# Optimization experiments

Measured on AMD Instinct MI355X. Metric: run time of the kernel, lower is better.

Reference implementation:

```python
import jax, jax.numpy as jnp
import numpy as np

B, S, D, H, L, DFF, NA = 128, 52, 1024, 16, 8, 4096, 1000
DK = D // H
KTOP = int((1.0 - 0.9) * S)  # per-row top-k kept before threshold = 5
EPS = 1e-5
SCALE = 1.0 / np.sqrt(DK).astype(np.float32)


def setup_inputs() -> dict:
    key = jax.random.key(0)
    ks = jax.random.split(key, 30)
    # token grid: channels 0,1 in [0,50) so only designated positions match special tokens
    x = jax.random.randint(ks[0], (B, S, 3), 0, 50).astype(jnp.int32)
    act = jax.random.randint(ks[1], (B, S), 0, NA).astype(jnp.int32)
    x = x.at[..., 2].set(act)
    x = x.at[:, 0].set(jnp.array([100, 0, 1], jnp.int32))    # SOS
    x = x.at[:, 26].set(jnp.array([100, 0, 2], jnp.int32))   # SEP
    x = x.at[:, 48:].set(jnp.array([100, 0, 0], jnp.int32))  # PAD tail

    def n(k, shape, scale=0.02):
        return (jax.random.normal(k, shape) * scale).astype(jnp.float32)

    return dict(
        x=x,
        action_emb=n(ks[2], (NA, D), 1.0),
        sep_token=n(ks[3], (D,), 1.0),
        bn_gamma=jnp.ones((S,), jnp.float32),
        bn_beta=jnp.zeros((S,), jnp.float32),
        Wq=n(ks[4], (L, D, D)), bq=jnp.zeros((L, D), jnp.float32),
        Wk=n(ks[5], (L, D, D)), bk=jnp.zeros((L, D), jnp.float32),
        Wv=n(ks[6], (L, D, D)), bv=jnp.zeros((L, D), jnp.float32),
        Wo=n(ks[7], (L, D, D)), bo=jnp.zeros((L, D), jnp.float32),
        W1=n(ks[8], (L, DFF, D)), b1=jnp.zeros((L, DFF), jnp.float32),
        W2=n(ks[9], (L, D, DFF)), b2=jnp.zeros((L, D), jnp.float32),
        ln1_g=jnp.ones((L, D), jnp.float32), ln1_b=jnp.zeros((L, D), jnp.float32),
        ln2_g=jnp.ones((L, D), jnp.float32), ln2_b=jnp.zeros((L, D), jnp.float32),
        Wout=n(ks[10], (3, D)), bout=jnp.zeros((3,), jnp.float32),
    )


def _ln(x, g, b):
    m = x.mean(-1, keepdims=True)
    v = x.var(-1, keepdims=True)
    return (x - m) * jax.lax.rsqrt(v + EPS) * g + b


def reference(x, action_emb, sep_token, bn_gamma, bn_beta,
              Wq, bq, Wk, bk, Wv, bv, Wo, bo,
              W1, b1, W2, b2, ln1_g, ln1_b, ln2_g, ln2_b, Wout, bout):
    PAD = jnp.array([100, 0, 0], x.dtype)
    SEP = jnp.array([100, 0, 2], x.dtype)
    pad = jnp.all(x == PAD, -1)            # [B,S]
    sep = jnp.all(x == SEP, -1)            # [B,S]
    valid = ~pad                            # attend only to non-pad keys

    # token-scatter embedding: sep positions -> sep_token, everything else -> action embedding
    h = jnp.where(sep[..., None], sep_token, action_emb[x[..., 2]])  # [B,S,D]

    # BatchNorm1d(52) over seq-as-channel dim (training-mode batch stats)
    mu = h.mean((0, 2), keepdims=True)
    var = h.var((0, 2), keepdims=True)
    h = (h - mu) * jax.lax.rsqrt(var + EPS) * bn_gamma[None, :, None] + bn_beta[None, :, None]

    for l in range(L):
        q = (h @ Wq[l].T + bq[l]).reshape(B, S, H, DK).transpose(0, 2, 1, 3)
        k = (h @ Wk[l].T + bk[l]).reshape(B, S, H, DK).transpose(0, 2, 1, 3)
        v = (h @ Wv[l].T + bv[l]).reshape(B, S, H, DK).transpose(0, 2, 1, 3)
        scores = jnp.einsum('bhqd,bhkd->bhqk', q, k) * SCALE       # [B,H,S,S]
        scores = jnp.where(valid[:, None, None, :], scores, -1e9)
        thr = jax.lax.top_k(scores, KTOP)[0][..., -1:]              # per-row k-th largest
        sparse = scores * (scores >= thr).astype(scores.dtype)      # zero out sub-threshold
        attn = jax.nn.softmax(sparse, axis=-1)
        o = jnp.einsum('bhqk,bhkd->bhqd', attn, v).transpose(0, 2, 1, 3).reshape(B, S, D)
        o = o @ Wo[l].T + bo[l]
        h = _ln(h + o, ln1_g[l], ln1_b[l])
        f = jax.nn.relu(h @ W1[l].T + b1[l]) @ W2[l].T + b2[l]
        h = _ln(h + f, ln2_g[l], ln2_b[l])

    y = h @ Wout.T + bout                                           # [B,S,3]
    return y[:, -1]
```

## Files before the change

kernel.cpp:

```cpp
#include <hip/hip_runtime.h>
#include <cstddef>
#include <cstdint>

#define B_    128
#define S_    52
#define D_    1024
#define H_    16
#define L_    8
#define DFF_  4096
#define DK_   64
#define T_    (B_*S_)
#define EPS_  1e-5f
#define SCALE_ 0.125f

typedef unsigned short ushortx4 __attribute__((ext_vector_type(4)));
typedef short  bf16x8 __attribute__((ext_vector_type(8)));
typedef float  f32x4  __attribute__((ext_vector_type(4)));

__device__ __forceinline__ unsigned short f2b(float f) {
  unsigned int u = __builtin_bit_cast(unsigned int, f);
  u = u + 0x7fffu + ((u >> 16) & 1u);
  return (unsigned short)(u >> 16);
}
__device__ __forceinline__ float b2f(unsigned short b) {
  unsigned int u = ((unsigned int)b) << 16;
  return __builtin_bit_cast(float, u);
}
__device__ __forceinline__ void gload16(const void* g, void* l) {
  __builtin_amdgcn_global_load_lds((const __attribute__((address_space(1))) unsigned int*)g,
      (__attribute__((address_space(3))) unsigned int*)l, 16, 0, 0);
}

__global__ __launch_bounds__(256) void k_embed(const int* __restrict__ x,
    const float* __restrict__ aemb, const float* __restrict__ sept,
    float* __restrict__ h, float* __restrict__ part, int* __restrict__ mask)
{
  int row = blockIdx.x;
  int b = row / S_;
  int s = row - b * S_;
  const int* xr = x + (size_t)row * 3;
  int x0 = xr[0], x1 = xr[1], x2 = xr[2];
  bool issep = (x0 == 100) && (x1 == 0) && (x2 == 2);
  bool ispad = (x0 == 100) && (x1 == 0) && (x2 == 0);
  int t = threadIdx.x;
  if (t == 0) mask[row] = ispad ? 0 : 1;
  const float* src = issep ? sept : (aemb + (size_t)x2 * D_);
  size_t base = (size_t)row * D_;
  float s1 = 0.f, s2 = 0.f;
#pragma unroll
  for (int i = 0; i < 4; ++i) {
    int d = t + i * 256;
    float v = src[d];
    h[base + d] = v;
    s1 += v;
    s2 += v * v;
  }
#pragma unroll
  for (int off = 32; off; off >>= 1) {
    s1 += __shfl_down(s1, off);
    s2 += __shfl_down(s2, off);
  }
  __shared__ float red[8];
  int lane = t & 63, wid = t >> 6;
  if (lane == 0) { red[wid] = s1; red[4 + wid] = s2; }
  __syncthreads();
  if (t == 0) {
    part[(size_t)s * B_ + b]        = red[0] + red[1] + red[2] + red[3];
    part[(size_t)(S_ + s) * B_ + b] = red[4] + red[5] + red[6] + red[7];
  }
}

__global__ __launch_bounds__(128) void k_bn_reduce(const float* __restrict__ part,
                                                   float* __restrict__ stats)
{
  int s = blockIdx.x;
  int t = threadIdx.x;
  float s1 = part[(size_t)s * B_ + t];
  float s2 = part[(size_t)(S_ + s) * B_ + t];
#pragma unroll
  for (int off = 32; off; off >>= 1) {
    s1 += __shfl_down(s1, off);
    s2 += __shfl_down(s2, off);
  }
  __shared__ float red[4];
  int lane = t & 63, wid = t >> 6;
  if (lane == 0) { red[wid] = s1; red[2 + wid] = s2; }
  __syncthreads();
  if (t == 0) {
    stats[s]      = red[0] + red[1];
    stats[S_ + s] = red[2] + red[3];
  }
}

__global__ __launch_bounds__(256) void k_bn_apply(float* __restrict__ h,
    const float* __restrict__ stats, const float* __restrict__ g,
    const float* __restrict__ bb, unsigned short* __restrict__ hb)
{
  int row = blockIdx.x;
  int s = row % S_;
  const float cnt = (float)(B_ * D_);
  float mu  = stats[s] / cnt;
  float var = stats[S_ + s] / cnt - mu * mu;
  float sc  = rsqrtf(var + EPS_) * g[s];
  float off = bb[s] - mu * sc;
  size_t base = (size_t)row * D_;
  int t = threadIdx.x;
#pragma unroll
  for (int i = 0; i < 4; ++i) {
    int d = t + i * 256;
    float v = h[base + d] * sc + off;
    h[base + d] = v;
    hb[base + d] = f2b(v);
  }
}

__global__ __launch_bounds__(256) void k_wconv8(
    const float* __restrict__ Wq, const float* __restrict__ Wk,
    const float* __restrict__ Wv, const float* __restrict__ Wo,
    const float* __restrict__ W1, const float* __restrict__ W2,
    unsigned short* __restrict__ out, int nlayers)
{
  const size_t DD = (size_t)D_ * D_;
  const size_t DF = (size_t)DFF_ * D_;
  const size_t per = 4 * DD + 2 * DF;
  const size_t total = per * (size_t)nlayers;
  size_t stride = (size_t)gridDim.x * 256 * 4;
  for (size_t i = ((size_t)blockIdx.x * 256 + threadIdx.x) * 4; i < total; i += stride) {
    size_t lay = i / per;
    size_t j = i - lay * per;
    const float* src; size_t off;
    if      (j < DD)          { src = Wq + lay * DD; off = j; }
    else if (j < 2 * DD)      { src = Wk + lay * DD; off = j - DD; }
    else if (j < 3 * DD)      { src = Wv + lay * DD; off = j - 2 * DD; }
    else if (j < 4 * DD)      { src = Wo + lay * DD; off = j - 3 * DD; }
    else if (j < 4 * DD + DF) { src = W1 + lay * DF; off = j - 4 * DD; }
    else                      { src = W2 + lay * DF; off = j - 4 * DD - DF; }
    float4 v = *reinterpret_cast<const float4*>(src + off);
    ushortx4 o = { f2b(v.x), f2b(v.y), f2b(v.z), f2b(v.w) };
    *reinterpret_cast<ushortx4*>(out + i) = o;
  }
}

__global__ __launch_bounds__(256) void k_bcat(const float* __restrict__ bq,
    const float* __restrict__ bk, const float* __restrict__ bv,
    float* __restrict__ out)
{
  int i = blockIdx.x * 256 + threadIdx.x;
  int l = i / 3072, j = i - l * 3072;
  float v = (j < D_) ? bq[l * D_ + j] : (j < 2 * D_) ? bk[l * D_ + j - D_]
                                                     : bv[l * D_ + j - 2 * D_];
  out[i] = v;
}

template<int RELU, int OUTBF16>
__global__ __launch_bounds__(512, 4) void k_gemm8(
    const unsigned short* __restrict__ A, const unsigned short* __restrict__ Wt,
    const float* __restrict__ bias, void* __restrict__ C,
    int Mtiles, int Ntiles, int K, int ldc)
{
  __shared__ unsigned short lds[3 * 12288];
  const int tid = threadIdx.x;
  const int w = tid >> 6, l = tid & 63;

  const int nwg = Mtiles * Ntiles;
  int id = blockIdx.x;
  int swz = (id & 7) * (nwg >> 3) + (id >> 3);
  const int stripe = swz / (Ntiles << 3);
  const int r = swz - stripe * (Ntiles << 3);
  int hg = Mtiles - (stripe << 3); if (hg > 8) hg = 8;
  const int c = r / (hg << 3);
  const int q = r - c * (hg << 3);
  const int bym = (stripe << 3) + (q >> 3);
  const int bxn = (c << 3) + (q & 7);
  const int bm = bym * 256, bn = bxn * 128;

  const int colsw = 16 * ((l & 3) ^ ((l >> 3) & 3));
  const char* gA = (const char*)A + ((size_t)(bm + w * 32 + (l >> 2)) * K) * 2 + colsw;
  const char* gB = (const char*)Wt + ((size_t)(bn + w * 16 + (l >> 2)) * K) * 2 + colsw;
  const size_t r16 = (size_t)16 * K * 2;
  unsigned short* lA = lds + w * 1024;
  unsigned short* lB = lds + 8192 + w * 512;

#define STAGE(tt, bb) do {                          \
    size_t ko_ = (size_t)(tt) * 64;                 \
    unsigned short* la_ = lA + (bb) * 12288;        \
    unsigned short* lb_ = lB + (bb) * 12288;        \
    gload16(gA + ko_,       la_);                   \
    gload16(gA + ko_ + r16, la_ + 512);             \
    gload16(gB + ko_,       lb_);                   \
  } while (0)

  const int fr = l & 15, kg = l >> 4;
  const int wr = w >> 1, wc = w & 1;
  const int xk = 16 * (kg ^ ((fr >> 1) & 3));
  const int aOff = (wr * 64 + fr) * 64 + xk;
  const int bOff = 16384 + (wc * 64 + fr) * 64 + xk;

  f32x4 acc[4][4] = {};
  const int NT = K >> 5;

  STAGE(0, 0);
  STAGE(1, 1);
  int cur = 0;
  for (int t = 0; t < NT; ++t) {
    if (t + 1 < NT) { asm volatile("s_waitcnt vmcnt(3)" ::: "memory"); }
    else            { asm volatile("s_waitcnt vmcnt(0)" ::: "memory"); }
    __builtin_amdgcn_sched_barrier(0);
    __builtin_amdgcn_s_barrier();
    __builtin_amdgcn_sched_barrier(0);
    if (t + 2 < NT) {
      int nb = cur + 2; if (nb >= 3) nb -= 3;
      STAGE(t + 2, nb);
    }
    const char* bp = (const char*)lds + cur * 24576;
    bf16x8 af[4], bfv[4];
#pragma unroll
    for (int mf = 0; mf < 4; ++mf)
      af[mf] = *(const bf16x8*)(bp + aOff + mf * 1024);
#pragma unroll
    for (int nf = 0; nf < 4; ++nf)
      bfv[nf] = *(const bf16x8*)(bp + bOff + nf * 1024);
    asm volatile("s_waitcnt lgkmcnt(0)" ::: "memory");
    __builtin_amdgcn_sched_barrier(0);
    __builtin_amdgcn_s_setprio(1);
#pragma unroll
    for (int mf = 0; mf < 4; ++mf)
#pragma unroll
      for (int nf = 0; nf < 4; ++nf)
        acc[mf][nf] = __builtin_amdgcn_mfma_f32_16x16x32_bf16(af[mf], bfv[nf], acc[mf][nf], 0, 0, 0);
    __builtin_amdgcn_s_setprio(0);
    __builtin_amdgcn_sched_barrier(0);
    cur = (cur == 2) ? 0 : cur + 1;
  }
#undef STAGE

#pragma unroll
  for (int nf = 0; nf < 4; ++nf) {
    int col = bn + wc * 64 + nf * 16 + fr;
    float bv = bias[col];
#pragma unroll
    for (int mf = 0; mf < 4; ++mf) {
      int row0 = bm + wr * 64 + mf * 16 + kg * 4;
#pragma unroll
      for (int j = 0; j < 4; ++j) {
        float v = acc[mf][nf][j] + bv;
        if (RELU) v = fmaxf(v, 0.f);
        if (OUTBF16)
          ((unsigned short*)C)[(size_t)(row0 + j) * ldc + col] = f2b(v);
        else
          ((float*)C)[(size_t)(row0 + j) * ldc + col] = v;
      }
    }
  }
}

__global__ __launch_bounds__(64) void k_attn(const unsigned short* __restrict__ qkv,
    const int* __restrict__ mask, unsigned short* __restrict__ ao)
{
  __shared__ float sc[64][68];
  __shared__ unsigned short ph[64][68];
  __shared__ unsigned short plo[64][68];
  __shared__ unsigned short vT[64][68];
  __shared__ float dnm[64];

  int blk = blockIdx.x;
  int b = blk >> 4, hh = blk & 15;
  int l = threadIdx.x;
  int cl = l & 15, kg = l >> 4;
  const unsigned short* base = qkv + (size_t)(b * S_) * 3072 + hh * 64;

  {
    const unsigned short* vp = base + 2048 + l;
#pragma unroll 4
    for (int k = 0; k < S_; ++k)
      vT[l][k] = vp[(size_t)k * 3072];
#pragma unroll
    for (int k = S_; k < 64; ++k) vT[l][k] = 0;
  }

  bf16x8 qa[4][2], kb[4][2];
#pragma unroll
  for (int mi = 0; mi < 4; ++mi) {
    int row = mi * 16 + cl;
    bool ok = (row < S_);
    const unsigned short* qp = base + (size_t)row * 3072 + kg * 8;
#pragma unroll
    for (int ks = 0; ks < 2; ++ks) {
      bf16x8 z = {};
      qa[mi][ks] = ok ? *reinterpret_cast<const bf16x8*>(qp + ks * 32) : z;
      kb[mi][ks] = ok ? *reinterpret_cast<const bf16x8*>(qp + 1024 + ks * 32) : z;
    }
  }

  f32x4 acc[4][4] = {};
#pragma unroll
  for (int ks = 0; ks < 2; ++ks)
#pragma unroll
    for (int mi = 0; mi < 4; ++mi)
#pragma unroll
      for (int ci = 0; ci < 4; ++ci)
        acc[mi][ci] = __builtin_amdgcn_mfma_f32_16x16x32_bf16(qa[mi][ks], kb[ci][ks], acc[mi][ci], 0, 0, 0);

  int vld[4];
#pragma unroll
  for (int ci = 0; ci < 4; ++ci) {
    int col = ci * 16 + cl;
    vld[ci] = (col < S_) ? mask[b * S_ + col] : 0;
  }
#pragma unroll
  for (int mi = 0; mi < 4; ++mi)
#pragma unroll
    for (int ci = 0; ci < 4; ++ci)
#pragma unroll
      for (int j = 0; j < 4; ++j)
        sc[mi * 16 + kg * 4 + j][ci * 16 + cl] = vld[ci] ? acc[mi][ci][j] * SCALE_ : -1e9f;

  __syncthreads();

  if (l < S_) {
    float v0 = -3e38f, v1 = -3e38f, v2 = -3e38f, v3 = -3e38f, v4 = -3e38f;
    const float4* rp = reinterpret_cast<const float4*>(&sc[l][0]);
#pragma unroll
    for (int c4 = 0; c4 < 13; ++c4) {
      float4 x = rp[c4];
      float xs[4] = { x.x, x.y, x.z, x.w };
#pragma unroll
      for (int u = 0; u < 4; ++u) {
        float xv = xs[u];
        if      (xv > v0) { v4 = v3; v3 = v2; v2 = v1; v1 = v0; v0 = xv; }
        else if (xv > v1) { v4 = v3; v3 = v2; v2 = v1; v1 = xv; }
        else if (xv > v2) { v4 = v3; v3 = v2; v2 = xv; }
        else if (xv > v3) { v4 = v3; v3 = xv; }
        else if (xv > v4) { v4 = xv; }
      }
    }
    float thr = v4;
    float m = fmaxf(v0, 0.f);
    float denom = 0.f;
    for (int c = 0; c < S_; ++c) {
      float xv = sc[l][c];
      float sp = (xv >= thr) ? xv : 0.f;
      float e = __expf(sp - m);
      denom += e;
      unsigned short hi = f2b(e);
      ph[l][c] = hi;
      plo[l][c] = f2b(e - b2f(hi));
    }
#pragma unroll
    for (int c = S_; c < 64; ++c) { ph[l][c] = 0; plo[l][c] = 0; }
    dnm[l] = 1.f / denom;
  }
  __syncthreads();

  f32x4 o[4][4] = {};
#pragma unroll
  for (int ks = 0; ks < 2; ++ks) {
    bf16x8 vf[4];
#pragma unroll
    for (int di = 0; di < 4; ++di)
      vf[di] = *reinterpret_cast<const bf16x8*>(&vT[di * 16 + cl][ks * 32 + kg * 8]);
#pragma unroll
    for (int mi = 0; mi < 4; ++mi) {
      bf16x8 ahi = *reinterpret_cast<const bf16x8*>(&ph[mi * 16 + cl][ks * 32 + kg * 8]);
      bf16x8 alo = *reinterpret_cast<const bf16x8*>(&plo[mi * 16 + cl][ks * 32 + kg * 8]);
#pragma unroll
      for (int di = 0; di < 4; ++di) {
        o[mi][di] = __builtin_amdgcn_mfma_f32_16x16x32_bf16(ahi, vf[di], o[mi][di], 0, 0, 0);
        o[mi][di] = __builtin_amdgcn_mfma_f32_16x16x32_bf16(alo, vf[di], o[mi][di], 0, 0, 0);
      }
    }
  }

#pragma unroll
  for (int mi = 0; mi < 4; ++mi) {
    int row = mi * 16 + kg * 4;
    if (row < S_) {
#pragma unroll
      for (int j = 0; j < 4; ++j) {
        int r = row + j;
        float inv = dnm[r];
        unsigned short* aop = ao + (size_t)(b * S_ + r) * D_ + hh * DK_;
#pragma unroll
        for (int di = 0; di < 4; ++di)
          aop[di * 16 + cl] = f2b(o[mi][di][j] * inv);
      }
    }
  }
}

__global__ __launch_bounds__(256) void k_add_ln(float* __restrict__ h,
    const float* __restrict__ r, const float* __restrict__ g,
    const float* __restrict__ bb, unsigned short* __restrict__ hb)
{
  int row = blockIdx.x;
  size_t base = (size_t)row * D_;
  int t = threadIdx.x;
  float xs[4];
  float s1 = 0.f, s2 = 0.f;
#pragma unroll
  for (int i = 0; i < 4; ++i) {
    int d = t + i * 256;
    float xv = h[base + d] + r[base + d];
    xs[i] = xv;
    s1 += xv;
    s2 += xv * xv;
  }
#pragma unroll
  for (int off = 32; off; off >>= 1) {
    s1 += __shfl_down(s1, off);
    s2 += __shfl_down(s2, off);
  }
  __shared__ float red[8];
  int lane = t & 63, wid = t >> 6;
  if (lane == 0) { red[wid] = s1; red[4 + wid] = s2; }
  __syncthreads();
  if (t == 0) {
    red[0] = red[0] + red[1] + red[2] + red[3];
    red[4] = red[4] + red[5] + red[6] + red[7];
  }
  __syncthreads();
  float mean = red[0] / (float)D_;
  float var  = red[4] / (float)D_ - mean * mean;
  float inv  = rsqrtf(var + EPS_);
#pragma unroll
  for (int i = 0; i < 4; ++i) {
    int d = t + i * 256;
    float v = (xs[i] - mean) * inv * g[d] + bb[d];
    h[base + d] = v;
    hb[base + d] = f2b(v);
  }
}

__global__ __launch_bounds__(256) void k_final(const float* __restrict__ h,
    const float* __restrict__ Wout, const float* __restrict__ bout,
    float* __restrict__ y)
{
  int b = blockIdx.x;
  const float* hr = h + (size_t)(b * S_ + (S_ - 1)) * D_;
  int t = threadIdx.x;
  float p0 = 0.f, p1 = 0.f, p2 = 0.f;
  for (int d = t; d < D_; d += 256) {
    float xv = hr[d];
    p0 += xv * Wout[d];
    p1 += xv * Wout[D_ + d];
    p2 += xv * Wout[2 * D_ + d];
  }
#pragma unroll
  for (int off = 32; off; off >>= 1) {
    p0 += __shfl_down(p0, off);
    p1 += __shfl_down(p1, off);
    p2 += __shfl_down(p2, off);
  }
  __shared__ float red[12];
  int lane = t & 63, wid = t >> 6;
  if (lane == 0) { red[wid] = p0; red[4 + wid] = p1; red[8 + wid] = p2; }
  __syncthreads();
  if (t == 0) {
    y[b * 3 + 0] = red[0] + red[1] + red[2]  + red[3]  + bout[0];
    y[b * 3 + 1] = red[4] + red[5] + red[6]  + red[7]  + bout[1];
    y[b * 3 + 2] = red[8] + red[9] + red[10] + red[11] + bout[2];
  }
}

extern "C" void kernel_launch(void* const* d_in, const int* in_sizes, int n_in,
                              void* d_out, int out_size, void* d_ws, size_t ws_size,
                              hipStream_t stream)
{
  const int*   x    = (const int*)d_in[0];
  const float* aemb = (const float*)d_in[1];
  const float* sept = (const float*)d_in[2];
  const float* bng  = (const float*)d_in[3];
  const float* bnb  = (const float*)d_in[4];
  const float* Wq = (const float*)d_in[5];  const float* bq = (const float*)d_in[6];
  const float* Wk = (const float*)d_in[7];  const float* bk = (const float*)d_in[8];
  const float* Wv = (const float*)d_in[9];  const float* bv = (const float*)d_in[10];
  const float* Wo = (const float*)d_in[11]; const float* bo = (const float*)d_in[12];
  const float* W1 = (const float*)d_in[13]; const float* b1 = (const float*)d_in[14];
  const float* W2 = (const float*)d_in[15]; const float* b2 = (const float*)d_in[16];
  const float* ln1g = (const float*)d_in[17]; const float* ln1b = (const float*)d_in[18];
  const float* ln2g = (const float*)d_in[19]; const float* ln2b = (const float*)d_in[20];
  const float* Wout = (const float*)d_in[21]; const float* bout = (const float*)d_in[22];
  float* out = (float*)d_out;

  float* ws = (float*)d_ws;
  const size_t TD = (size_t)T_ * D_;
  const size_t DD = (size_t)D_ * D_;
  const size_t DF = (size_t)DFF_ * D_;
  const size_t WPL = 4 * DD + 2 * DF;
  float* h   = ws;
  float* tmp = ws + TD;
  unsigned short* hb   = (unsigned short*)(ws + 2 * TD);
  unsigned short* qkvb = (unsigned short*)(ws + 2 * TD + TD / 2);
  unsigned short* aob  = (unsigned short*)(ws + 4 * TD);
  unsigned short* ffb  = (unsigned short*)(ws + 4 * TD + TD / 2);
  float* bqkv  = ws + 6 * TD + TD / 2;
  float* stats = bqkv + L_ * 3072;
  float* part  = stats + 2 * S_;
  int*   mask  = (int*)(part + 2 * S_ * B_);
  size_t usedB = ((char*)(mask + T_) - (char*)ws + 255) & ~(size_t)255;
  unsigned short* wbuf = (unsigned short*)((char*)ws + usedB);
  const int all8 = (ws_size >= usedB + 8 * WPL * sizeof(unsigned short)) ? 1 : 0;

  k_embed<<<T_, 256, 0, stream>>>(x, aemb, sept, h, part, mask);
  k_bn_reduce<<<S_, 128, 0, stream>>>(part, stats);
  k_bn_apply<<<T_, 256, 0, stream>>>(h, stats, bng, bnb, hb);
  k_bcat<<<(L_ * 3072) / 256, 256, 0, stream>>>(bq, bk, bv, bqkv);
  if (all8)
    k_wconv8<<<4096, 256, 0, stream>>>(Wq, Wk, Wv, Wo, W1, W2, wbuf, L_);

  for (int l = 0; l < L_; ++l) {
    unsigned short* wl = all8 ? (wbuf + (size_t)l * WPL) : wbuf;
    if (!all8)
      k_wconv8<<<3072, 256, 0, stream>>>(Wq + l * DD, Wk + l * DD, Wv + l * DD,
                                         Wo + l * DD, W1 + l * DF, W2 + l * DF, wbuf, 1);
    k_gemm8<0, 1><<<26 * 24, 512, 0, stream>>>(hb, wl, bqkv + l * 3072,
        qkvb, 26, 24, 1024, 3072);
    k_attn<<<B_ * H_, 64, 0, stream>>>(qkvb, mask, aob);
    k_gemm8<0, 0><<<26 * 8, 512, 0, stream>>>(aob, wl + 3 * DD, bo + l * D_,
        tmp, 26, 8, 1024, 1024);
    k_add_ln<<<T_, 256, 0, stream>>>(h, tmp, ln1g + l * D_, ln1b + l * D_, hb);
    k_gemm8<1, 1><<<26 * 32, 512, 0, stream>>>(hb, wl + 4 * DD, b1 + l * DFF_,
        ffb, 26, 32, 1024, 4096);
    k_gemm8<0, 0><<<26 * 8, 512, 0, stream>>>(ffb, wl + 4 * DD + DF, b2 + l * D_,
        tmp, 26, 8, 4096, 1024);
    k_add_ln<<<T_, 256, 0, stream>>>(h, tmp, ln2g + l * D_, ln2b + l * D_, hb);
  }
  k_final<<<B_, 256, 0, stream>>>(h, Wout, bout, out);
}
```

Measured before the change: 2.438 ms.

## Add 256x256 tiled pipelined GEMM for QKV and FFN1; split weight conversion by segment

```diff
diff --git a/kernel.cpp b/kernel.cpp
--- a/kernel.cpp
+++ b/kernel.cpp
@@ -114,30 +114,30 @@
   }
 }
 
-__global__ __launch_bounds__(256) void k_wconv8(
+__global__ __launch_bounds__(256) void k_wconv6(
     const float* __restrict__ Wq, const float* __restrict__ Wk,
     const float* __restrict__ Wv, const float* __restrict__ Wo,
     const float* __restrict__ W1, const float* __restrict__ W2,
-    unsigned short* __restrict__ out, int nlayers)
-{
-  const size_t DD = (size_t)D_ * D_;
-  const size_t DF = (size_t)DFF_ * D_;
-  const size_t per = 4 * DD + 2 * DF;
-  const size_t total = per * (size_t)nlayers;
+    unsigned short* __restrict__ out)
+{
+  const size_t DD = (size_t)D_ * D_, DF = (size_t)DFF_ * D_;
+  const size_t WPL = 4 * DD + 2 * DF;
+  int s = blockIdx.y, l = blockIdx.z;
+  const float* src; size_t segsz, dstoff;
+  switch (s) {
+    case 0:  src = Wq + (size_t)l * DD; segsz = DD; dstoff = 0; break;
+    case 1:  src = Wk + (size_t)l * DD; segsz = DD; dstoff = DD; break;
+    case 2:  src = Wv + (size_t)l * DD; segsz = DD; dstoff = 2 * DD; break;
+    case 3:  src = Wo + (size_t)l * DD; segsz = DD; dstoff = 3 * DD; break;
+    case 4:  src = W1 + (size_t)l * DF; segsz = DF; dstoff = 4 * DD; break;
+    default: src = W2 + (size_t)l * DF; segsz = DF; dstoff = 4 * DD + DF; break;
+  }
+  unsigned short* dst = out + (size_t)l * WPL + dstoff;
   size_t stride = (size_t)gridDim.x * 256 * 4;
-  for (size_t i = ((size_t)blockIdx.x * 256 + threadIdx.x) * 4; i < total; i += stride) {
-    size_t lay = i / per;
-    size_t j = i - lay * per;
-    const float* src; size_t off;
-    if      (j < DD)          { src = Wq + lay * DD; off = j; }
-    else if (j < 2 * DD)      { src = Wk + lay * DD; off = j - DD; }
-    else if (j < 3 * DD)      { src = Wv + lay * DD; off = j - 2 * DD; }
-    else if (j < 4 * DD)      { src = Wo + lay * DD; off = j - 3 * DD; }
-    else if (j < 4 * DD + DF) { src = W1 + lay * DF; off = j - 4 * DD; }
-    else                      { src = W2 + lay * DF; off = j - 4 * DD - DF; }
-    float4 v = *reinterpret_cast<const float4*>(src + off);
+  for (size_t i = ((size_t)blockIdx.x * 256 + threadIdx.x) * 4; i < segsz; i += stride) {
+    float4 v = *reinterpret_cast<const float4*>(src + i);
     ushortx4 o = { f2b(v.x), f2b(v.y), f2b(v.z), f2b(v.w) };
-    *reinterpret_cast<ushortx4*>(out + i) = o;
+    *reinterpret_cast<ushortx4*>(dst + i) = o;
   }
 }
 
@@ -150,6 +150,141 @@
   float v = (j < D_) ? bq[l * D_ + j] : (j < 2 * D_) ? bk[l * D_ + j - D_]
                                                      : bv[l * D_ + j - 2 * D_];
   out[i] = v;
+}
+
+template<int RELU, int OUTBF16>
+__global__ __launch_bounds__(512) void k_gemm256(
+    const unsigned short* __restrict__ A, const unsigned short* __restrict__ Wt,
+    const float* __restrict__ bias, void* __restrict__ C,
+    int Mtiles, int Ntiles, int K, int ldc)
+{
+  __shared__ char lds[2 * 65536];
+  const int tid = threadIdx.x;
+  const int w = tid >> 6, lane = tid & 63;
+  const int wm = w >> 2, wn = w & 3;
+  const int fr = lane & 15, kg = lane >> 4;
+
+  const int nwg = Mtiles * Ntiles;
+  int id = blockIdx.x;
+  int swz = (id & 7) * (nwg >> 3) + (id >> 3);
+  const int stripe = swz / (Ntiles << 3);
+  const int rrem = swz - stripe * (Ntiles << 3);
+  int hg = Mtiles - (stripe << 3); if (hg > 8) hg = 8;
+  const int cc = rrem / (hg << 2);
+  const int qq = rrem - cc * (hg << 2);
+  const int bym = (stripe << 3) + (qq >> 2);
+  const int bxn = (cc << 2) + (qq & 3);
+  const int bm = bym * 256, bn = bxn * 256;
+
+  const size_t Kb = (size_t)K * 2;
+  const size_t r128 = (size_t)128 * Kb;
+  const size_t rh64 = (size_t)64 * Kb;
+  const size_t ch32 = (size_t)32 * Kb;
+  const int swz16 = ((tid & 7) ^ ((tid >> 3) & 7)) << 4;
+  const char* gA0 = (const char*)A + (size_t)(bm + (tid >> 3)) * Kb + swz16;
+  const char* gB0 = (const char*)Wt +
+      (size_t)(bn + (((tid >> 8) & 1) << 6) + ((tid >> 3) & 31)) * Kb + swz16;
+  char* dA = lds + w * 1024;
+  char* dB = lds + 32768 + w * 1024;
+
+#define STG_A(kt, rh, db) do {                                       \
+    size_t ko_ = (size_t)(kt) * 128 + (size_t)(rh) * rh64;           \
+    gload16(gA0 + ko_,        dA + (db) * 65536 + (rh) * 16384);     \
+    gload16(gA0 + ko_ + r128, dA + (db) * 65536 + (rh) * 16384 + 8192); \
+  } while (0)
+#define STG_B(kt, ch, db) do {                                       \
+    size_t ko_ = (size_t)(kt) * 128 + (size_t)(ch) * ch32;           \
+    gload16(gB0 + ko_,        dB + (db) * 65536 + (ch) * 16384);     \
+    gload16(gB0 + ko_ + r128, dB + (db) * 65536 + (ch) * 16384 + 8192); \
+  } while (0)
+
+  f32x4 acc[8][4] = {};
+  bf16x8 a[4][2], b0[2][2], b1[2][2];
+
+#define DSR_A(rh, db) do {                                           \
+  _Pragma("unroll") for (int q_ = 0; q_ < 4; ++q_)                   \
+  _Pragma("unroll") for (int ks_ = 0; ks_ < 2; ++ks_)                \
+    a[q_][ks_] = *(const bf16x8*)(lds + (db) * 65536 +               \
+      ((rh) * 128 + wm * 64 + q_ * 16 + fr) * 128 +                  \
+      (((ks_ * 4 + kg) ^ (fr & 7)) << 4));                           \
+} while (0)
+#define DSR_B(ch, dst, db) do {                                      \
+  _Pragma("unroll") for (int cf_ = 0; cf_ < 2; ++cf_)                \
+  _Pragma("unroll") for (int ks_ = 0; ks_ < 2; ++ks_)                \
+    dst[cf_][ks_] = *(const bf16x8*)(lds + (db) * 65536 + 32768 +    \
+      ((ch) * 128 + wn * 32 + cf_ * 16 + fr) * 128 +                 \
+      (((ks_ * 4 + kg) ^ (fr & 7)) << 4));                           \
+} while (0)
+#define MFMA16(rh, ch, bsrc) do {                                    \
+  _Pragma("unroll") for (int q_ = 0; q_ < 4; ++q_)                   \
+  _Pragma("unroll") for (int cf_ = 0; cf_ < 2; ++cf_)                \
+  _Pragma("unroll") for (int ks_ = 0; ks_ < 2; ++ks_)                \
+    acc[(rh) * 4 + q_][(ch) * 2 + cf_] =                             \
+      __builtin_amdgcn_mfma_f32_16x16x32_bf16(a[q_][ks_],            \
+        bsrc[cf_][ks_], acc[(rh) * 4 + q_][(ch) * 2 + cf_], 0, 0, 0);\
+} while (0)
+#define BAR() do { __builtin_amdgcn_sched_barrier(0);                \
+  __builtin_amdgcn_s_barrier(); __builtin_amdgcn_sched_barrier(0); } while (0)
+#define MCL(rh, ch, bsrc) do {                                       \
+  asm volatile("s_waitcnt lgkmcnt(0)" ::: "memory");                 \
+  __builtin_amdgcn_sched_barrier(0);                                 \
+  __builtin_amdgcn_s_setprio(1);                                     \
+  MFMA16(rh, ch, bsrc);                                              \
+  __builtin_amdgcn_s_setprio(0);                                     \
+  __builtin_amdgcn_sched_barrier(0); } while (0)
+
+  const int NKT = K >> 6;
+  STG_A(0, 0, 0); STG_B(0, 0, 0); STG_B(0, 1, 0); STG_A(0, 1, 0);
+  STG_A(1, 0, 1); STG_B(1, 0, 1); STG_B(1, 1, 1); STG_A(1, 1, 1);
+  asm volatile("s_waitcnt vmcnt(0)" ::: "memory");
+  BAR();
+
+  for (int kt = 0; kt < NKT; ++kt) {
+    const int db = kt & 1;
+    const bool s2 = (kt + 2 < NKT);
+    DSR_A(0, db); DSR_B(0, b0, db);
+    if (kt >= 1 && kt + 1 < NKT) STG_A(kt + 1, 1, db ^ 1);
+    BAR(); MCL(0, 0, b0); BAR();
+    DSR_B(1, b1, db);
+    if (s2) STG_A(kt + 2, 0, db);
+    BAR(); MCL(0, 1, b1); BAR();
+    DSR_A(1, db);
+    if (s2) STG_B(kt + 2, 0, db);
+    BAR(); MCL(1, 1, b1); BAR();
+    if (s2) {
+      STG_B(kt + 2, 1, db);
+      asm volatile("s_waitcnt vmcnt(6)" ::: "memory");
+    } else {
+      asm volatile("s_waitcnt vmcnt(0)" ::: "memory");
+    }
+    BAR(); MCL(1, 0, b0); BAR();
+  }
+#undef STG_A
+#undef STG_B
+#undef DSR_A
+#undef DSR_B
+#undef MFMA16
+#undef BAR
+#undef MCL
+
+#pragma unroll
+  for (int RF = 0; RF < 8; ++RF) {
+    int row0 = bm + wm * 128 + RF * 16 + kg * 4;
+#pragma unroll
+    for (int CF = 0; CF < 4; ++CF) {
+      int col = bn + wn * 64 + CF * 16 + fr;
+      float bv = bias[col];
+#pragma unroll
+      for (int j = 0; j < 4; ++j) {
+        float v = acc[RF][CF][j] + bv;
+        if (RELU) v = fmaxf(v, 0.f);
+        if (OUTBF16)
+          ((unsigned short*)C)[(size_t)(row0 + j) * ldc + col] = f2b(v);
+        else
+          ((float*)C)[(size_t)(row0 + j) * ldc + col] = v;
+      }
+    }
+  }
 }
 
 template<int RELU, int OUTBF16>
@@ -506,21 +641,21 @@
   k_bn_apply<<<T_, 256, 0, stream>>>(h, stats, bng, bnb, hb);
   k_bcat<<<(L_ * 3072) / 256, 256, 0, stream>>>(bq, bk, bv, bqkv);
   if (all8)
-    k_wconv8<<<4096, 256, 0, stream>>>(Wq, Wk, Wv, Wo, W1, W2, wbuf, L_);
+    k_wconv6<<<dim3(96, 6, 8), 256, 0, stream>>>(Wq, Wk, Wv, Wo, W1, W2, wbuf);
 
   for (int l = 0; l < L_; ++l) {
     unsigned short* wl = all8 ? (wbuf + (size_t)l * WPL) : wbuf;
     if (!all8)
-      k_wconv8<<<3072, 256, 0, stream>>>(Wq + l * DD, Wk + l * DD, Wv + l * DD,
-                                         Wo + l * DD, W1 + l * DF, W2 + l * DF, wbuf, 1);
-    k_gemm8<0, 1><<<26 * 24, 512, 0, stream>>>(hb, wl, bqkv + l * 3072,
-        qkvb, 26, 24, 1024, 3072);
+      k_wconv6<<<dim3(96, 6, 1), 256, 0, stream>>>(Wq + l * DD, Wk + l * DD,
+          Wv + l * DD, Wo + l * DD, W1 + l * DF, W2 + l * DF, wbuf);
+    k_gemm256<0, 1><<<26 * 12, 512, 0, stream>>>(hb, wl, bqkv + l * 3072,
+        qkvb, 26, 12, 1024, 3072);
     k_attn<<<B_ * H_, 64, 0, stream>>>(qkvb, mask, aob);
     k_gemm8<0, 0><<<26 * 8, 512, 0, stream>>>(aob, wl + 3 * DD, bo + l * D_,
         tmp, 26, 8, 1024, 1024);
     k_add_ln<<<T_, 256, 0, stream>>>(h, tmp, ln1g + l * D_, ln1b + l * D_, hb);
-    k_gemm8<1, 1><<<26 * 32, 512, 0, stream>>>(hb, wl + 4 * DD, b1 + l * DFF_,
-        ffb, 26, 32, 1024, 4096);
+    k_gemm256<1, 1><<<26 * 16, 512, 0, stream>>>(hb, wl + 4 * DD, b1 + l * DFF_,
+        ffb, 26, 16, 1024, 4096);
     k_gemm8<0, 0><<<26 * 8, 512, 0, stream>>>(ffb, wl + 4 * DD + DF, b2 + l * D_,
         tmp, 26, 8, 4096, 1024);
     k_add_ln<<<T_, 256, 0, stream>>>(h, tmp, ln2g + l * D_, ln2b + l * D_, hb);
```

After: 2.571 ms. 1.05x slower.
